# Optimization experiments

Measured on AMD Instinct MI355X. Metric: run time of the kernel, lower is better.

## Reference

```python
import jax, jax.numpy as jnp
import numpy as np
from jax import lax

B = 256; N_LAB = 20000; M = 3; D = 768
T = 5; K = 8; H = 256; DI = 512; S = 16; R = 16; NL = 4; KC = 4


def setup_inputs() -> dict:
    key = jax.random.key(0)
    ks = jax.random.split(key, 16)
    sc = 0.02
    return {
        "unlabeled_embeddings": jax.random.normal(ks[0], (B, M, D), jnp.float32),
        "labeled_embeddings": jax.random.normal(ks[1], (N_LAB, M, D), jnp.float32),
        "labeled_traits": jax.random.uniform(ks[2], (N_LAB, T), jnp.float32),
        "modality_logits": jax.random.normal(ks[3], (T, M), jnp.float32),
        "Wp": jax.random.normal(ks[4], (D + 1, H), jnp.float32) * sc,
        "bp": jnp.zeros((H,), jnp.float32),
        "ln_g": jnp.ones((NL, H), jnp.float32),
        "ln_b": jnp.zeros((NL, H), jnp.float32),
        "Win": jax.random.normal(ks[5], (NL, H, 2 * DI), jnp.float32) * sc,
        "conv_w": jax.random.normal(ks[6], (NL, DI, KC), jnp.float32) * sc,
        "conv_b": jnp.zeros((NL, DI), jnp.float32),
        "Wx": jax.random.normal(ks[7], (NL, DI, R + 2 * S), jnp.float32) * sc,
        "Wdt": jax.random.normal(ks[8], (NL, R, DI), jnp.float32) * sc,
        "bdt": jnp.full((NL, DI), -4.6, jnp.float32),
        "A_log": jnp.log(jnp.broadcast_to(jnp.arange(1, S + 1, dtype=jnp.float32), (NL, DI, S))),
        "Dp": jnp.ones((NL, DI), jnp.float32),
        "Wout": jax.random.normal(ks[9], (NL, DI, H), jnp.float32) * sc,
        "W1": jax.random.normal(ks[10], (H, H // 2), jnp.float32) * sc,
        "b1": jnp.zeros((H // 2,), jnp.float32),
        "W2": jax.random.normal(ks[11], (H // 2, 1), jnp.float32) * sc,
        "b2": jnp.zeros((1,), jnp.float32),
    }


def layer_norm(x, g, b, eps=1e-5):
    m = x.mean(-1, keepdims=True)
    v = ((x - m) ** 2).mean(-1, keepdims=True)
    return (x - m) * lax.rsqrt(v + eps) * g + b


def select_neighbors(lab_e, lab_t, unl_e, mlog):
    # Per-trait modality-weighted cosine similarity k-NN.
    w = jax.nn.softmax(mlog, axis=-1)                       # (T,M)
    q = jnp.einsum('tm,bmd->btd', w, unl_e)                 # (B,T,D)
    kk = jnp.einsum('tm,nmd->ntd', w, lab_e)                # (N,T,D)
    qn = q * lax.rsqrt(jnp.sum(q * q, -1, keepdims=True) + 1e-8)
    kn = kk * lax.rsqrt(jnp.sum(kk * kk, -1, keepdims=True) + 1e-8)
    sim = jnp.einsum('btd,ntd->btn', qn, kn)                # (B,T,N)
    _, idx = lax.top_k(sim, K)                              # (B,T,K) int32
    ne = lab_e[idx]                                         # (B,T,K,M,D)
    tg = lab_t[idx]                                         # (B,T,K,T)
    nt = jnp.diagonal(tg, axis1=1, axis2=3).transpose(0, 2, 1)  # (B,T,K)
    return ne, nt, idx


def mamba_block(x, Win, conv_w, conv_b, Wx, Wdt, bdt, A_log, Dp, Wout):
    # x: (N, L, H). Selective SSM (Mamba) block with internal residual.
    N, L, _ = x.shape
    xz = x @ Win                                            # (N,L,2*DI)
    xc, z = jnp.split(xz, 2, axis=-1)
    xp = jnp.pad(xc, ((0, 0), (KC - 1, 0), (0, 0)))         # causal depthwise conv, k=4
    xc = sum(xp[:, j:j + L, :] * conv_w[:, j] for j in range(KC)) + conv_b
    xc = jax.nn.silu(xc)
    dbl = xc @ Wx                                           # (N,L,R+2S)
    dt, Bm, Cm = jnp.split(dbl, [R, R + S], axis=-1)
    dt = jax.nn.softplus(dt @ Wdt + bdt)                    # (N,L,DI)
    A = -jnp.exp(A_log)                                     # (DI,S)
    dA = jnp.exp(dt[..., None] * A)                         # (N,L,DI,S)
    dBx = dt[..., None] * Bm[:, :, None, :] * xc[..., None] # (N,L,DI,S)

    def step(h, inp):
        a, bx = inp
        h = a * h + bx
        return h, h

    h0 = jnp.zeros((N, DI, S), x.dtype)
    _, hs = lax.scan(step, h0, (jnp.swapaxes(dA, 0, 1), jnp.swapaxes(dBx, 0, 1)))
    hs = jnp.swapaxes(hs, 0, 1)                             # (N,L,DI,S)
    y = jnp.einsum('nlds,nls->nld', hs, Cm) + Dp * xc
    y = y * jax.nn.silu(z)
    return x + y @ Wout


def _forward(unl, lab_e, lab_t, mlog, Wp, bp, ln_g, ln_b, Win, conv_w, conv_b, Wx,
             Wdt, bdt, A_log, Dp, Wout, W1, b1, W2, b2):
    ne, nt, _ = select_neighbors(lab_e, lab_t, unl, mlog)
    ne = ne.mean(3)                                         # (B,T,K,D) mean over modalities
    uc = unl.mean(1)                                        # (B,D)
    feats = jnp.concatenate([ne, jnp.broadcast_to(uc[:, None, None, :], (B, T, 1, D))], axis=2)
    tt = jnp.concatenate([nt[..., None], jnp.zeros((B, T, 1, 1), lab_t.dtype)], axis=2)
    toks = jnp.concatenate([feats, tt], axis=-1).reshape(B * T, K + 1, D + 1)
    x = toks @ Wp + bp                                      # (B*T, K+1, H)
    for i in range(NL):
        xn = layer_norm(x, ln_g[i], ln_b[i])
        x = mamba_block(xn, Win[i], conv_w[i], conv_b[i], Wx[i], Wdt[i], bdt[i],
                        A_log[i], Dp[i], Wout[i])
    ms = x[:, -1, :]                                        # masked-trait token state
    h1 = jax.nn.relu(ms @ W1 + b1)
    return (h1 @ W2 + b2).reshape(B, T)


def reference(unlabeled_embeddings, labeled_embeddings, labeled_traits, modality_logits,
              Wp, bp, ln_g, ln_b, Win, conv_w, conv_b, Wx, Wdt, bdt, A_log, Dp, Wout,
              W1, b1, W2, b2):
    return _forward(unlabeled_embeddings, labeled_embeddings, labeled_traits,
                    modality_logits, Wp, bp, ln_g, ln_b, Win, conv_w, conv_b, Wx,
                    Wdt, bdt, A_log, Dp, Wout, W1, b1, W2, b2)
```

## Files before the change

### kernel.cpp

```cpp
#include <hip/hip_runtime.h>
#include <math.h>

#define B_   256
#define NLAB 20000
#define M_   3
#define D_   768
#define T_   5
#define K_   8
#define H_   256
#define DI_  512
#define S_   16
#define R_   16
#define NL_  4
#define KC_  4
#define L_   9
#define NBT  1280
#define NROW 11520

typedef __attribute__((ext_vector_type(8))) short bf16x8;
typedef __attribute__((ext_vector_type(4))) float floatx4;


__device__ __forceinline__ float block_reduce_sum(float v) {
    __shared__ float red[4];
    int lane = threadIdx.x & 63;
    int wid  = threadIdx.x >> 6;
#pragma unroll
    for (int o = 32; o > 0; o >>= 1) v += __shfl_down(v, o);
    if (lane == 0) red[wid] = v;
    __syncthreads();
    int nw = (int)(blockDim.x >> 6);
    float r = 0.f;
#pragma unroll
    for (int i = 0; i < 4; ++i) if (i < nw) r += red[i];
    __syncthreads();
    return r;
}

__device__ __forceinline__ float sigmoidf_(float x) { return 1.f / (1.f + expf(-x)); }
__device__ __forceinline__ float siluf_(float x)    { return x * sigmoidf_(x); }
__device__ __forceinline__ float softplusf_(float x){ return x > 20.f ? x : log1pf(expf(x)); }

__device__ __forceinline__ unsigned short f2bf(float x) {
    unsigned u = __float_as_uint(x);
    unsigned r = (u + 0x7fffu + ((u >> 16) & 1u)) >> 16;
    return (unsigned short)r;
}
__device__ __forceinline__ float bf2f(unsigned short h) {
    return __uint_as_float(((unsigned)h) << 16);
}

__device__ __forceinline__ void barrier_lds_only() {
    asm volatile("s_waitcnt lgkmcnt(0)" ::: "memory");
    __builtin_amdgcn_s_barrier();
}


__global__ void k_softmax_w(const float* __restrict__ mlog, float* __restrict__ w) {
    int t = threadIdx.x;
    if (t < T_) {
        float a = mlog[t*M_+0], b = mlog[t*M_+1], c = mlog[t*M_+2];
        float mx = fmaxf(a, fmaxf(b, c));
        float ea = expf(a-mx), eb = expf(b-mx), ec = expf(c-mx);
        float s = ea + eb + ec;
        w[t*M_+0] = ea/s; w[t*M_+1] = eb/s; w[t*M_+2] = ec/s;
    }
}

__global__ __launch_bounds__(256) void k_qn_uc(const float* __restrict__ unl,
                                               const float* __restrict__ w,
                                               unsigned short* __restrict__ qnh,
                                               unsigned short* __restrict__ qnl,
                                               float* __restrict__ uc) {
    int b = blockIdx.x, tid = threadIdx.x;
    float e[3][3];
#pragma unroll
    for (int c = 0; c < 3; ++c) {
        int d = tid + c*256;
#pragma unroll
        for (int m = 0; m < 3; ++m)
            e[c][m] = unl[((size_t)b*3 + m)*D_ + d];
    }
#pragma unroll
    for (int c = 0; c < 3; ++c)
        uc[(size_t)b*D_ + tid + c*256] = (e[c][0] + e[c][1] + e[c][2]) * (1.f/3.f);
    for (int t = 0; t < T_; ++t) {
        float w0 = w[t*3+0], w1 = w[t*3+1], w2 = w[t*3+2];
        float q[3]; float ss = 0.f;
#pragma unroll
        for (int c = 0; c < 3; ++c) {
            q[c] = w0*e[c][0] + w1*e[c][1] + w2*e[c][2];
            ss += q[c]*q[c];
        }
        float tot = block_reduce_sum(ss);
        float inv = rsqrtf(tot + 1e-8f);
#pragma unroll
        for (int c = 0; c < 3; ++c) {
            float v = q[c]*inv;
            size_t o = ((size_t)t*B_ + b)*D_ + tid + c*256;
            unsigned short h = f2bf(v);
            qnh[o] = h; qnl[o] = f2bf(v - bf2f(h));
        }
    }
}

__device__ __forceinline__ void cvt_store4(const float4* rb, float w0, float w1, float w2,
                                           unsigned short* bh, unsigned short* bl,
                                           int off, float& ss) {
    float4 s;
    s.x = w0*rb[0].x + w1*rb[1].x + w2*rb[2].x;
    s.y = w0*rb[0].y + w1*rb[1].y + w2*rb[2].y;
    s.z = w0*rb[0].z + w1*rb[1].z + w2*rb[2].z;
    s.w = w0*rb[0].w + w1*rb[1].w + w2*rb[2].w;
    ss += s.x*s.x + s.y*s.y + s.z*s.z + s.w*s.w;
    ushort4 h, l;
    h.x = f2bf(s.x); l.x = f2bf(s.x - bf2f(h.x));
    h.y = f2bf(s.y); l.y = f2bf(s.y - bf2f(h.y));
    h.z = f2bf(s.z); l.z = f2bf(s.z - bf2f(h.z));
    h.w = f2bf(s.w); l.w = f2bf(s.w - bf2f(h.w));
    *(ushort4*)(bh + off) = h;
    *(ushort4*)(bl + off) = l;
}

__global__ __launch_bounds__(512, 4) void k_simf(const unsigned short* __restrict__ qnh,
                                                 const unsigned short* __restrict__ qnl,
                                                 const float* __restrict__ lab_e,
                                                 const float* __restrict__ w,
                                                 float* __restrict__ sim) {
    __shared__ unsigned short Ah[2][128*36], Al[2][128*36];
    __shared__ unsigned short Bh[2][128*36], Bl[2][128*36];
    __shared__ float rnl[128];

    int bid = blockIdx.x;
    int xcd = bid & 7, s = bid >> 3;
    int cnt = (xcd < 5) ? 20 : 19;
    if (s >= cnt * 10) return;
    int start = (xcd < 5) ? xcd*20 : 100 + (xcd - 5)*19;
    int chunk = start + s / 10;
    int inner = s - (s / 10) * 10;
    int mch = inner / 5;
    int t = inner - mch * 5;
    int bn = chunk * 128;
    int bm = mch * 128;

    float w0 = w[t*3+0], w1 = w[t*3+1], w2 = w[t*3+2];
    int tid = threadIdx.x;
    int lane = tid & 63, wv = tid >> 6;
    int mbase = (wv >> 2)*64, nbase = (wv & 3)*32;
    int fr = lane & 15, kg = lane >> 4;

    int ar = tid >> 2, akq = tid & 3;
    const unsigned short* agh = qnh + ((size_t)t*B_ + bm + ar)*D_ + akq*8;
    const unsigned short* agl = qnl + ((size_t)t*B_ + bm + ar)*D_ + akq*8;
    int aoff = ar*36 + akq*8;

    int gr0 = tid >> 3, gr1 = 64 + (tid >> 3), kq = tid & 7;
    int gn0 = bn + gr0, gn1 = bn + gr1;
    bool v0 = gn0 < NLAB, v1 = gn1 < NLAB;
    const float* bp0 = lab_e + (size_t)gn0*(3*D_) + kq*4;
    const float* bp1 = lab_e + (size_t)gn1*(3*D_) + kq*4;
    int soff0 = gr0*36 + kq*4, soff1 = gr1*36 + kq*4;

    floatx4 acc[4][2];
#pragma unroll
    for (int mi = 0; mi < 4; ++mi)
#pragma unroll
        for (int ni = 0; ni < 2; ++ni)
            acc[mi][ni] = (floatx4){0.f, 0.f, 0.f, 0.f};

    float ss0 = 0.f, ss1 = 0.f;
    float4 rb0[3], rb1[3];
    float4 z4 = make_float4(0.f, 0.f, 0.f, 0.f);
    int4 lah, lal;

    rb0[0]=rb0[1]=rb0[2]=z4; rb1[0]=rb1[1]=rb1[2]=z4;
    if (v0) { rb0[0] = *(const float4*)(bp0);
              rb0[1] = *(const float4*)(bp0 + D_);
              rb0[2] = *(const float4*)(bp0 + 2*D_); }
    if (v1) { rb1[0] = *(const float4*)(bp1);
              rb1[1] = *(const float4*)(bp1 + D_);
              rb1[2] = *(const float4*)(bp1 + 2*D_); }
    lah = *(const int4*)(agh);
    lal = *(const int4*)(agl);

    *(int4*)(&Ah[0][aoff]) = lah;
    *(int4*)(&Al[0][aoff]) = lal;
    cvt_store4(rb0, w0, w1, w2, &Bh[0][0], &Bl[0][0], soff0, ss0);
    cvt_store4(rb1, w0, w1, w2, &Bh[0][0], &Bl[0][0], soff1, ss1);

    if (v0) { rb0[0] = *(const float4*)(bp0 + 32);
              rb0[1] = *(const float4*)(bp0 + D_ + 32);
              rb0[2] = *(const float4*)(bp0 + 2*D_ + 32); }
    if (v1) { rb1[0] = *(const float4*)(bp1 + 32);
              rb1[1] = *(const float4*)(bp1 + D_ + 32);
              rb1[2] = *(const float4*)(bp1 + 2*D_ + 32); }
    lah = *(const int4*)(agh + 32);
    lal = *(const int4*)(agl + 32);

    for (int kt = 0; kt < 24; ++kt) {
        int cur = kt & 1;
        barrier_lds_only();

        bf16x8 bhf[2], blf[2];
#pragma unroll
        for (int ni = 0; ni < 2; ++ni) {
            int off = (nbase + ni*16 + fr)*36 + kg*8;
            bhf[ni] = *(const bf16x8*)(&Bh[cur][off]);
            blf[ni] = *(const bf16x8*)(&Bl[cur][off]);
        }
#pragma unroll
        for (int mi = 0; mi < 4; ++mi) {
            int off = (mbase + mi*16 + fr)*36 + kg*8;
            bf16x8 ahf = *(const bf16x8*)(&Ah[cur][off]);
            bf16x8 alf = *(const bf16x8*)(&Al[cur][off]);
#pragma unroll
            for (int ni = 0; ni < 2; ++ni) {
                floatx4 c = acc[mi][ni];
                c = __builtin_amdgcn_mfma_f32_16x16x32_bf16(ahf, bhf[ni], c, 0, 0, 0);
                c = __builtin_amdgcn_mfma_f32_16x16x32_bf16(alf, bhf[ni], c, 0, 0, 0);
                c = __builtin_amdgcn_mfma_f32_16x16x32_bf16(ahf, blf[ni], c, 0, 0, 0);
                acc[mi][ni] = c;
            }
        }
        if (kt < 23) {
            int nxt = cur ^ 1;
            *(int4*)(&Ah[nxt][aoff]) = lah;
            *(int4*)(&Al[nxt][aoff]) = lal;
            cvt_store4(rb0, w0, w1, w2, &Bh[nxt][0], &Bl[nxt][0], soff0, ss0);
            cvt_store4(rb1, w0, w1, w2, &Bh[nxt][0], &Bl[nxt][0], soff1, ss1);
            if (kt < 22) {
                int k2 = (kt + 2) * 32;
                if (v0) { rb0[0] = *(const float4*)(bp0 + k2);
                          rb0[1] = *(const float4*)(bp0 + D_ + k2);
                          rb0[2] = *(const float4*)(bp0 + 2*D_ + k2); }
                if (v1) { rb1[0] = *(const float4*)(bp1 + k2);
                          rb1[1] = *(const float4*)(bp1 + D_ + k2);
                          rb1[2] = *(const float4*)(bp1 + 2*D_ + k2); }
                lah = *(const int4*)(agh + k2);
                lal = *(const int4*)(agl + k2);
            }
        }
    }

    float t0 = ss0, t1 = ss1;
#pragma unroll
    for (int m = 1; m <= 4; m <<= 1) { t0 += __shfl_xor(t0, m); t1 += __shfl_xor(t1, m); }
    if ((tid & 7) == 0) {
        rnl[tid >> 3]        = rsqrtf(t0 + 1e-8f);
        rnl[64 + (tid >> 3)] = rsqrtf(t1 + 1e-8f);
    }
    __syncthreads();

    float* st = sim + (size_t)t*B_*NLAB;
#pragma unroll
    for (int mi = 0; mi < 4; ++mi) {
        int m = bm + mbase + mi*16 + kg*4;
#pragma unroll
        for (int ni = 0; ni < 2; ++ni) {
            int nl = nbase + ni*16 + fr;
            int n = bn + nl;
            if (n < NLAB) {
                float rv = rnl[nl];
#pragma unroll
                for (int r2 = 0; r2 < 4; ++r2)
                    st[(size_t)(m + r2)*NLAB + n] = acc[mi][ni][r2] * rv;
            }
        }
    }
}

__global__ __launch_bounds__(256) void k_topk(const float* __restrict__ sim,
                                              int* __restrict__ idx_out) {
    int b = blockIdx.x;
    int t = blockIdx.y;
    int tid = threadIdx.x;
    const float* row = sim + ((size_t)t*B_ + b)*NLAB;
    float tv[8]; int ti[8];
#pragma unroll
    for (int k = 0; k < 8; ++k) { tv[k] = -3e38f; ti[k] = 0x7fffffff; }
    for (int n = tid; n < NLAB; n += 256) {
        float v = row[n];
        if (v > tv[7]) {
            tv[7] = v; ti[7] = n;
#pragma unroll
            for (int k = 7; k > 0; --k) {
                if (tv[k] > tv[k-1]) {
                    float fv = tv[k]; tv[k] = tv[k-1]; tv[k-1] = fv;
                    int fi = ti[k]; ti[k] = ti[k-1]; ti[k-1] = fi;
                }
            }
        }
    }
    __shared__ float sv[2048];
    __shared__ int   si[2048];
    __shared__ float pv[256];
    __shared__ int   pi[256];
    __shared__ int   pp[256];
#pragma unroll
    for (int k = 0; k < 8; ++k) { sv[tid*8+k] = tv[k]; si[tid*8+k] = ti[k]; }
    __syncthreads();
    for (int r = 0; r < 8; ++r) {
        float bv = -3e38f; int bi = 0x7fffffff; int bp = 0;
#pragma unroll
        for (int k = 0; k < 8; ++k) {
            int p = tid*8 + k;
            float v = sv[p]; int ii = si[p];
            if (v > bv || (v == bv && ii < bi)) { bv = v; bi = ii; bp = p; }
        }
        pv[tid] = bv; pi[tid] = bi; pp[tid] = bp;
        __syncthreads();
        for (int off = 128; off > 0; off >>= 1) {
            if (tid < off) {
                if (pv[tid+off] > pv[tid] || (pv[tid+off] == pv[tid] && pi[tid+off] < pi[tid])) {
                    pv[tid] = pv[tid+off]; pi[tid] = pi[tid+off]; pp[tid] = pp[tid+off];
                }
            }
            __syncthreads();
        }
        if (tid == 0) {
            idx_out[((size_t)b*T_ + t)*K_ + r] = pi[0];
            sv[pp[0]] = -3e38f;
        }
        __syncthreads();
    }
}

__global__ __launch_bounds__(256) void k_toks(const float* __restrict__ lab_e,
                                              const float* __restrict__ lab_t,
                                              const float* __restrict__ uc,
                                              const int* __restrict__ idx,
                                              unsigned short* __restrict__ tokh,
                                              unsigned short* __restrict__ tokl,
                                              float* __restrict__ tt) {
    int g = blockIdx.x;
    int bt = g / L_, l = g % L_;
    int b = bt / T_, t = bt % T_;
    size_t ro = (size_t)g*D_;
    if (l < K_) {
        int n = idx[(size_t)bt*K_ + l];
        for (int d = threadIdx.x; d < D_; d += 256) {
            size_t base = (size_t)n*(3*D_) + d;
            float v = (lab_e[base] + lab_e[base + D_] + lab_e[base + 2*D_]) * (1.f/3.f);
            unsigned short h = f2bf(v);
            tokh[ro + d] = h; tokl[ro + d] = f2bf(v - bf2f(h));
        }
        if (threadIdx.x == 0) tt[g] = lab_t[(size_t)n*T_ + t];
    } else {
        for (int d = threadIdx.x; d < D_; d += 256) {
            float v = uc[(size_t)b*D_ + d];
            unsigned short h = f2bf(v);
            tokh[ro + d] = h; tokl[ro + d] = f2bf(v - bf2f(h));
        }
        if (threadIdx.x == 0) tt[g] = 0.f;
    }
}

__global__ void k_cvtw(const float* __restrict__ W,
                       unsigned short* __restrict__ th,
                       unsigned short* __restrict__ tl,
                       int Kd, int N) {
    int total = Kd * N;
    for (int id = blockIdx.x*256 + threadIdx.x; id < total; id += gridDim.x*256) {
        int n = id / Kd, k = id - n*Kd;
        float v = W[(size_t)k*N + n];
        unsigned short h = f2bf(v);
        th[id] = h; tl[id] = f2bf(v - bf2f(h));
    }
}

template<bool ADD, bool BIAS, bool TRAIT>
__global__ __launch_bounds__(256) void k_mgemm(const unsigned short* __restrict__ ah,
                                               const unsigned short* __restrict__ al,
                                               const unsigned short* __restrict__ bh,
                                               const unsigned short* __restrict__ bl,
                                               const float* __restrict__ bias,
                                               const float* __restrict__ wtrait,
                                               const float* __restrict__ tt,
                                               float* __restrict__ C,
                                               int N, int Kd) {
    __shared__ unsigned short Ah[128*40], Al[128*40], Bh[64*40], Bl[64*40];
    int bn = blockIdx.x * 64;
    int bm = blockIdx.y * 128;
    int tid = threadIdx.x;
    int lane = tid & 63, wv = tid >> 6;
    int mbase = (wv >> 1)*64, nbase = (wv & 1)*32;
    int fr = lane & 15, kg = lane >> 4;
    floatx4 acc[4][2];
#pragma unroll
    for (int mi = 0; mi < 4; ++mi)
#pragma unroll
        for (int ni = 0; ni < 2; ++ni)
            acc[mi][ni] = (floatx4){0.f, 0.f, 0.f, 0.f};

    for (int k0 = 0; k0 < Kd; k0 += 32) {
#pragma unroll
        for (int f = 0; f < 2; ++f) {
            int v = f*256 + tid;
            int r = v >> 2, kq = v & 3;
            size_t g = (size_t)(bm + r)*Kd + k0 + kq*8;
            int off = r*40 + kq*8;
            *(int4*)(Ah + off) = *(const int4*)(ah + g);
            *(int4*)(Al + off) = *(const int4*)(al + g);
        }
        {
            int r = tid >> 2, kq = tid & 3;
            size_t g = (size_t)(bn + r)*Kd + k0 + kq*8;
            int off = r*40 + kq*8;
            *(int4*)(Bh + off) = *(const int4*)(bh + g);
            *(int4*)(Bl + off) = *(const int4*)(bl + g);
        }
        __syncthreads();

        bf16x8 bhf[2], blf[2];
#pragma unroll
        for (int ni = 0; ni < 2; ++ni) {
            int off = (nbase + ni*16 + fr)*40 + kg*8;
            bhf[ni] = *(const bf16x8*)(Bh + off);
            blf[ni] = *(const bf16x8*)(Bl + off);
        }
#pragma unroll
        for (int mi = 0; mi < 4; ++mi) {
            int off = (mbase + mi*16 + fr)*40 + kg*8;
            bf16x8 ahf = *(const bf16x8*)(Ah + off);
            bf16x8 alf = *(const bf16x8*)(Al + off);
#pragma unroll
            for (int ni = 0; ni < 2; ++ni) {
                floatx4 c = acc[mi][ni];
                c = __builtin_amdgcn_mfma_f32_16x16x32_bf16(ahf, bhf[ni], c, 0, 0, 0);
                c = __builtin_amdgcn_mfma_f32_16x16x32_bf16(alf, bhf[ni], c, 0, 0, 0);
                c = __builtin_amdgcn_mfma_f32_16x16x32_bf16(ahf, blf[ni], c, 0, 0, 0);
                acc[mi][ni] = c;
            }
        }
        __syncthreads();
    }
#pragma unroll
    for (int mi = 0; mi < 4; ++mi) {
        int m0 = bm + mbase + mi*16 + kg*4;
#pragma unroll
        for (int ni = 0; ni < 2; ++ni) {
            int n = bn + nbase + ni*16 + fr;
#pragma unroll
            for (int r = 0; r < 4; ++r) {
                float v = acc[mi][ni][r];
                if (TRAIT) v += tt[m0 + r] * wtrait[n];
                if (BIAS)  v += bias[n];
                size_t o = (size_t)(m0 + r)*N + n;
                if (ADD) C[o] += v; else C[o] = v;
            }
        }
    }
}

__global__ __launch_bounds__(256) void k_ln(const float* __restrict__ x,
                                            const float* __restrict__ g,
                                            const float* __restrict__ b,
                                            float* __restrict__ xn,
                                            unsigned short* __restrict__ xnh,
                                            unsigned short* __restrict__ xnl) {
    int row = blockIdx.x, tid = threadIdx.x;
    float v = x[(size_t)row*H_ + tid];
    float mean = block_reduce_sum(v) * (1.f/H_);
    float d = v - mean;
    float var = block_reduce_sum(d*d) * (1.f/H_);
    float o = d * rsqrtf(var + 1e-5f) * g[tid] + b[tid];
    size_t oo = (size_t)row*H_ + tid;
    xn[oo] = o;
    unsigned short h = f2bf(o);
    xnh[oo] = h; xnl[oo] = f2bf(o - bf2f(h));
}

__global__ __launch_bounds__(512) void k_mamba(const float* __restrict__ xz,
                                               const float* __restrict__ cw,
                                               const float* __restrict__ cb,
                                               const unsigned short* __restrict__ wxh,
                                               const unsigned short* __restrict__ wxl,
                                               const float* __restrict__ Wdt,
                                               const float* __restrict__ bdt,
                                               const float* __restrict__ A_log,
                                               const float* __restrict__ Dp,
                                               unsigned short* __restrict__ yh,
                                               unsigned short* __restrict__ yl) {
    __shared__ float xcS[L_][516];
    __shared__ float dblS[L_][48];
    int n = blockIdx.x, d = threadIdx.x;

    float c0 = cw[d*4+0], c1 = cw[d*4+1], c2 = cw[d*4+2], c3 = cw[d*4+3];
    float bb = cb[d];
    const float* src = xz + (size_t)n*L_*(2*DI_) + d;
    float xc[L_], z[L_];
    float x0 = 0.f, x1 = 0.f, x2 = 0.f;
#pragma unroll
    for (int l = 0; l < L_; ++l) {
        float x3 = src[l*(2*DI_)];
        z[l]     = src[l*(2*DI_) + DI_];
        float s = bb + c0*x0 + c1*x1 + c2*x2 + c3*x3;
        float v = siluf_(s);
        xc[l] = v; xcS[l][d] = v;
        x0 = x1; x1 = x2; x2 = x3;
    }
    __syncthreads();

    int wv = d >> 6, lane = d & 63;
    if (wv < 3) {
        int fr = lane & 15, kg = lane >> 4;
        const unsigned short* bph = wxh + (size_t)(wv*16 + fr)*DI_;
        const unsigned short* bpl = wxl + (size_t)(wv*16 + fr)*DI_;
        floatx4 c = (floatx4){0.f, 0.f, 0.f, 0.f};
        for (int k0 = 0; k0 < DI_; k0 += 32) {
            int kb = k0 + kg*8;
            float av[8];
            if (fr < L_) {
                float4 q0 = *(const float4*)(&xcS[fr][kb]);
                float4 q1 = *(const float4*)(&xcS[fr][kb+4]);
                av[0]=q0.x; av[1]=q0.y; av[2]=q0.z; av[3]=q0.w;
                av[4]=q1.x; av[5]=q1.y; av[6]=q1.z; av[7]=q1.w;
            } else {
#pragma unroll
                for (int j = 0; j < 8; ++j) av[j] = 0.f;
            }
            bf16x8 ah, al;
#pragma unroll
            for (int j = 0; j < 8; ++j) {
                unsigned short hh = f2bf(av[j]);
                ah[j] = (short)hh;
                al[j] = (short)f2bf(av[j] - bf2f(hh));
            }
            bf16x8 bhf = *(const bf16x8*)(bph + kb);
            bf16x8 blf = *(const bf16x8*)(bpl + kb);
            c = __builtin_amdgcn_mfma_f32_16x16x32_bf16(ah, bhf, c, 0, 0, 0);
            c = __builtin_amdgcn_mfma_f32_16x16x32_bf16(al, bhf, c, 0, 0, 0);
            c = __builtin_amdgcn_mfma_f32_16x16x32_bf16(ah, blf, c, 0, 0, 0);
        }
#pragma unroll
        for (int r = 0; r < 4; ++r) {
            int row = kg*4 + r;
            if (row < L_) dblS[row][wv*16 + fr] = c[r];
        }
    }
    __syncthreads();

    float a[S_], wdt[R_];
#pragma unroll
    for (int s = 0; s < S_; ++s) a[s] = -expf(A_log[(size_t)d*S_ + s]);
#pragma unroll
    for (int r = 0; r < R_; ++r) wdt[r] = Wdt[(size_t)r*DI_ + d];
    float bdtv = bdt[d], dp = Dp[d];
    float h[S_];
#pragma unroll
    for (int s = 0; s < S_; ++s) h[s] = 0.f;
    size_t ob = (size_t)n*L_*DI_ + d;
#pragma unroll
    for (int l = 0; l < L_; ++l) {
        float s = bdtv;
#pragma unroll
        for (int r = 0; r < R_; ++r) s = fmaf(dblS[l][r], wdt[r], s);
        float dtv = softplusf_(s);
        float xcv = xc[l];
        float accv = 0.f;
#pragma unroll
        for (int si = 0; si < S_; ++si) {
            float Bv = dblS[l][16 + si], Cv = dblS[l][32 + si];
            h[si] = expf(dtv*a[si])*h[si] + dtv*Bv*xcv;
            accv = fmaf(h[si], Cv, accv);
        }
        float yv = (accv + dp*xcv) * siluf_(z[l]);
        unsigned short hh = f2bf(yv);
        yh[ob + (size_t)l*DI_] = hh;
        yl[ob + (size_t)l*DI_] = f2bf(yv - bf2f(hh));
    }
}

__global__ __launch_bounds__(128) void k_head(const float* __restrict__ x,
                                              const float* __restrict__ W1,
                                              const float* __restrict__ b1,
                                              const float* __restrict__ W2,
                                              const float* __restrict__ b2,
                                              float* __restrict__ out) {
    int n = blockIdx.x, tid = threadIdx.x;
    __shared__ float ms[H_];
    const float* src = x + ((size_t)n*L_ + (L_-1))*H_;
    ms[tid] = src[tid];
    ms[tid+128] = src[tid+128];
    __syncthreads();
    float s = b1[tid];
#pragma unroll 8
    for (int k = 0; k < H_; ++k) s = fmaf(ms[k], W1[(size_t)k*128 + tid], s);
    float h = fmaxf(s, 0.f);
    float p = h * W2[tid];
    float tot = block_reduce_sum(p);
    if (tid == 0) out[n] = tot + b2[0];
}


extern "C" void kernel_launch(void* const* d_in, const int* in_sizes, int n_in,
                              void* d_out, int out_size, void* d_ws, size_t ws_size,
                              hipStream_t stream) {
    const float* unl   = (const float*)d_in[0];
    const float* lab_e = (const float*)d_in[1];
    const float* lab_t = (const float*)d_in[2];
    const float* mlog  = (const float*)d_in[3];
    const float* Wp    = (const float*)d_in[4];
    const float* bp    = (const float*)d_in[5];
    const float* ln_g  = (const float*)d_in[6];
    const float* ln_b  = (const float*)d_in[7];
    const float* Win   = (const float*)d_in[8];
    const float* conv_w= (const float*)d_in[9];
    const float* conv_b= (const float*)d_in[10];
    const float* Wx    = (const float*)d_in[11];
    const float* Wdt   = (const float*)d_in[12];
    const float* bdt   = (const float*)d_in[13];
    const float* A_log = (const float*)d_in[14];
    const float* Dp    = (const float*)d_in[15];
    const float* Wout  = (const float*)d_in[16];
    const float* W1    = (const float*)d_in[17];
    const float* b1    = (const float*)d_in[18];
    const float* W2    = (const float*)d_in[19];
    const float* b2    = (const float*)d_in[20];

    float* ws = (float*)d_ws;
    float* w    = ws + 0;
    int*   idx  = (int*)(ws + 16);
    float* uc   = ws + 10256;
    unsigned short* wxth = (unsigned short*)(ws + 206864);
    unsigned short* wxtl = (unsigned short*)(ws + 256016);
    float* tt   = ws + 306864;
    unsigned short* qnh   = (unsigned short*)(ws + 318384);
    unsigned short* qnl   = (unsigned short*)(ws + 809904);
    unsigned short* wph   = (unsigned short*)(ws + 1301424);
    unsigned short* wpl   = (unsigned short*)(ws + 1399728);
    unsigned short* winh  = (unsigned short*)(ws + 1498032);
    unsigned short* winl  = (unsigned short*)(ws + 2022320);
    unsigned short* wouth = (unsigned short*)(ws + 2546608);
    unsigned short* woutl = (unsigned short*)(ws + 2808752);
    float* xa   = ws + 3070896;
    float* xb   = ws + 6020016;
    unsigned short* xnh   = (unsigned short*)(ws + 8969136);
    unsigned short* xnl   = (unsigned short*)(ws + 10443696);
    float* simreg = ws + 18369456;
    float* sim  = simreg;
    float* xz   = simreg;
    unsigned short* tokh = (unsigned short*)(simreg + 11796480);
    unsigned short* tokl = (unsigned short*)(simreg + 16220160);
    unsigned short* yh   = (unsigned short*)(simreg + 17694720);
    unsigned short* yl   = (unsigned short*)(simreg + 20643840);

    k_softmax_w<<<1, 64, 0, stream>>>(mlog, w);
    k_qn_uc<<<B_, 256, 0, stream>>>(unl, w, qnh, qnl, uc);
    k_cvtw<<<(768*256 + 255)/256, 256, 0, stream>>>(Wp, wph, wpl, 768, 256);
    for (int i = 0; i < NL_; ++i) {
        k_cvtw<<<(256*1024 + 255)/256, 256, 0, stream>>>(Win + (size_t)i*H_*(2*DI_),
                                                         winh + (size_t)i*H_*(2*DI_),
                                                         winl + (size_t)i*H_*(2*DI_), 256, 1024);
        k_cvtw<<<(512*256 + 255)/256, 256, 0, stream>>>(Wout + (size_t)i*DI_*H_,
                                                        wouth + (size_t)i*DI_*H_,
                                                        woutl + (size_t)i*DI_*H_, 512, 256);
        k_cvtw<<<(512*48 + 255)/256, 256, 0, stream>>>(Wx + (size_t)i*DI_*48,
                                                       wxth + (size_t)i*48*DI_,
                                                       wxtl + (size_t)i*48*DI_, 512, 48);
    }
    k_simf<<<1600, 512, 0, stream>>>(qnh, qnl, lab_e, w, sim);
    {
        dim3 g(B_, T_);
        k_topk<<<g, 256, 0, stream>>>(sim, idx);
    }
    k_toks<<<NROW, 256, 0, stream>>>(lab_e, lab_t, uc, idx, tokh, tokl, tt);
    {
        dim3 g(H_/64, NROW/128);
        k_mgemm<false,true,true><<<g, 256, 0, stream>>>(tokh, tokl, wph, wpl,
                                                        bp, Wp + (size_t)768*H_, tt, xa, H_, D_);
    }
    float* cur = xa;
    float* oth = xb;
    for (int i = 0; i < NL_; ++i) {
        k_ln<<<NROW, 256, 0, stream>>>(cur, ln_g + (size_t)i*H_, ln_b + (size_t)i*H_, oth, xnh, xnl);
        {
            dim3 g((2*DI_)/64, NROW/128);
            k_mgemm<false,false,false><<<g, 256, 0, stream>>>(xnh, xnl,
                winh + (size_t)i*H_*(2*DI_), winl + (size_t)i*H_*(2*DI_),
                nullptr, nullptr, nullptr, xz, 2*DI_, H_);
        }
        k_mamba<<<NBT, 512, 0, stream>>>(xz,
                                         conv_w + (size_t)i*DI_*KC_, conv_b + (size_t)i*DI_,
                                         wxth + (size_t)i*48*DI_, wxtl + (size_t)i*48*DI_,
                                         Wdt + (size_t)i*R_*DI_, bdt + (size_t)i*DI_,
                                         A_log + (size_t)i*DI_*S_, Dp + (size_t)i*DI_,
                                         yh, yl);
        {
            dim3 g(H_/64, NROW/128);
            k_mgemm<true,false,false><<<g, 256, 0, stream>>>(yh, yl,
                wouth + (size_t)i*DI_*H_, woutl + (size_t)i*DI_*H_,
                nullptr, nullptr, nullptr, oth, H_, DI_);
        }
        float* tmp = cur; cur = oth; oth = tmp;
    }
    k_head<<<NBT, 128, 0, stream>>>(cur, W1, b1, W2, b2, (float*)d_out);
}
```

Before: 1.417 ms.

## Single-buffer LDS in similarity GEMM, pad rows to 40, raise occupancy

Replaces the double-buffered LDS tiles in the similarity GEMM with a single buffer and adds a second barrier per k-step, so the next tile's stores happen before compute rather than overlapping it. LDS row stride changes from 36 to 40 halves and launch bounds ask for 8 blocks per CU instead of 4. The bf16 conversions now use the compiler's native __bf16 cast. The aim is higher occupancy from the smaller LDS footprint, paid for with an extra barrier per k-step, less overlap inside each block, and possible register pressure at the higher occupancy target.

```diff
diff --git a/kernel.cpp b/kernel.cpp
--- a/kernel.cpp
+++ b/kernel.cpp
@@ -42,12 +42,10 @@
 __device__ __forceinline__ float softplusf_(float x){ return x > 20.f ? x : log1pf(expf(x)); }
 
 __device__ __forceinline__ unsigned short f2bf(float x) {
-    unsigned u = __float_as_uint(x);
-    unsigned r = (u + 0x7fffu + ((u >> 16) & 1u)) >> 16;
-    return (unsigned short)r;
+    return __builtin_bit_cast(unsigned short, (__bf16)x);
 }
 __device__ __forceinline__ float bf2f(unsigned short h) {
-    return __uint_as_float(((unsigned)h) << 16);
+    return (float)__builtin_bit_cast(__bf16, h);
 }
 
 __device__ __forceinline__ void barrier_lds_only() {
@@ -122,22 +120,22 @@
     *(ushort4*)(bl + off) = l;
 }
 
-__global__ __launch_bounds__(512, 4) void k_simf(const unsigned short* __restrict__ qnh,
+__global__ __launch_bounds__(512, 8) void k_simf(const unsigned short* __restrict__ qnh,
                                                  const unsigned short* __restrict__ qnl,
                                                  const float* __restrict__ lab_e,
                                                  const float* __restrict__ w,
                                                  float* __restrict__ sim) {
-    __shared__ unsigned short Ah[2][128*36], Al[2][128*36];
-    __shared__ unsigned short Bh[2][128*36], Bl[2][128*36];
+    __shared__ unsigned short Ah[128*40], Al[128*40];
+    __shared__ unsigned short Bh[128*40], Bl[128*40];
     __shared__ float rnl[128];
 
     int bid = blockIdx.x;
-    int xcd = bid & 7, s = bid >> 3;
+    int xcd = bid & 7, sb = bid >> 3;
     int cnt = (xcd < 5) ? 20 : 19;
-    if (s >= cnt * 10) return;
+    if (sb >= cnt * 10) return;
     int start = (xcd < 5) ? xcd*20 : 100 + (xcd - 5)*19;
-    int chunk = start + s / 10;
-    int inner = s - (s / 10) * 10;
+    int chunk = start + sb / 10;
+    int inner = sb - (sb / 10) * 10;
     int mch = inner / 5;
     int t = inner - mch * 5;
     int bn = chunk * 128;
@@ -152,14 +150,14 @@
     int ar = tid >> 2, akq = tid & 3;
     const unsigned short* agh = qnh + ((size_t)t*B_ + bm + ar)*D_ + akq*8;
     const unsigned short* agl = qnl + ((size_t)t*B_ + bm + ar)*D_ + akq*8;
-    int aoff = ar*36 + akq*8;
+    int aoff = ar*40 + akq*8;
 
     int gr0 = tid >> 3, gr1 = 64 + (tid >> 3), kq = tid & 7;
     int gn0 = bn + gr0, gn1 = bn + gr1;
     bool v0 = gn0 < NLAB, v1 = gn1 < NLAB;
     const float* bp0 = lab_e + (size_t)gn0*(3*D_) + kq*4;
     const float* bp1 = lab_e + (size_t)gn1*(3*D_) + kq*4;
-    int soff0 = gr0*36 + kq*4, soff1 = gr1*36 + kq*4;
+    int soff0 = gr0*40 + kq*4, soff1 = gr1*40 + kq*4;
 
     floatx4 acc[4][2];
 #pragma unroll
@@ -183,36 +181,40 @@
     lah = *(const int4*)(agh);
     lal = *(const int4*)(agl);
 
-    *(int4*)(&Ah[0][aoff]) = lah;
-    *(int4*)(&Al[0][aoff]) = lal;
-    cvt_store4(rb0, w0, w1, w2, &Bh[0][0], &Bl[0][0], soff0, ss0);
-    cvt_store4(rb1, w0, w1, w2, &Bh[0][0], &Bl[0][0], soff1, ss1);
-
-    if (v0) { rb0[0] = *(const float4*)(bp0 + 32);
-              rb0[1] = *(const float4*)(bp0 + D_ + 32);
-              rb0[2] = *(const float4*)(bp0 + 2*D_ + 32); }
-    if (v1) { rb1[0] = *(const float4*)(bp1 + 32);
-              rb1[1] = *(const float4*)(bp1 + D_ + 32);
-              rb1[2] = *(const float4*)(bp1 + 2*D_ + 32); }
-    lah = *(const int4*)(agh + 32);
-    lal = *(const int4*)(agl + 32);
-
     for (int kt = 0; kt < 24; ++kt) {
-        int cur = kt & 1;
         barrier_lds_only();
 
+        *(int4*)(&Ah[aoff]) = lah;
+        *(int4*)(&Al[aoff]) = lal;
+        cvt_store4(rb0, w0, w1, w2, Bh, Bl, soff0, ss0);
+        cvt_store4(rb1, w0, w1, w2, Bh, Bl, soff1, ss1);
+
+        if (kt < 23) {
+            int k2 = (kt + 1) * 32;
+            if (v0) { rb0[0] = *(const float4*)(bp0 + k2);
+                      rb0[1] = *(const float4*)(bp0 + D_ + k2);
+                      rb0[2] = *(const float4*)(bp0 + 2*D_ + k2); }
+            if (v1) { rb1[0] = *(const float4*)(bp1 + k2);
+                      rb1[1] = *(const float4*)(bp1 + D_ + k2);
+                      rb1[2] = *(const float4*)(bp1 + 2*D_ + k2); }
+            lah = *(const int4*)(agh + k2);
+            lal = *(const int4*)(agl + k2);
+        }
+
+        barrier_lds_only();
+
         bf16x8 bhf[2], blf[2];
 #pragma unroll
         for (int ni = 0; ni < 2; ++ni) {
-            int off = (nbase + ni*16 + fr)*36 + kg*8;
-            bhf[ni] = *(const bf16x8*)(&Bh[cur][off]);
-            blf[ni] = *(const bf16x8*)(&Bl[cur][off]);
+            int off = (nbase + ni*16 + fr)*40 + kg*8;
+            bhf[ni] = *(const bf16x8*)(Bh + off);
+            blf[ni] = *(const bf16x8*)(Bl + off);
         }
 #pragma unroll
         for (int mi = 0; mi < 4; ++mi) {
-            int off = (mbase + mi*16 + fr)*36 + kg*8;
-            bf16x8 ahf = *(const bf16x8*)(&Ah[cur][off]);
-            bf16x8 alf = *(const bf16x8*)(&Al[cur][off]);
+            int off = (mbase + mi*16 + fr)*40 + kg*8;
+            bf16x8 ahf = *(const bf16x8*)(Ah + off);
+            bf16x8 alf = *(const bf16x8*)(Al + off);
 #pragma unroll
             for (int ni = 0; ni < 2; ++ni) {
                 floatx4 c = acc[mi][ni];
@@ -220,24 +222,6 @@
                 c = __builtin_amdgcn_mfma_f32_16x16x32_bf16(alf, bhf[ni], c, 0, 0, 0);
                 c = __builtin_amdgcn_mfma_f32_16x16x32_bf16(ahf, blf[ni], c, 0, 0, 0);
                 acc[mi][ni] = c;
-            }
-        }
-        if (kt < 23) {
-            int nxt = cur ^ 1;
-            *(int4*)(&Ah[nxt][aoff]) = lah;
-            *(int4*)(&Al[nxt][aoff]) = lal;
-            cvt_store4(rb0, w0, w1, w2, &Bh[nxt][0], &Bl[nxt][0], soff0, ss0);
-            cvt_store4(rb1, w0, w1, w2, &Bh[nxt][0], &Bl[nxt][0], soff1, ss1);
-            if (kt < 22) {
-                int k2 = (kt + 2) * 32;
-                if (v0) { rb0[0] = *(const float4*)(bp0 + k2);
-                          rb0[1] = *(const float4*)(bp0 + D_ + k2);
-                          rb0[2] = *(const float4*)(bp0 + 2*D_ + k2); }
-                if (v1) { rb1[0] = *(const float4*)(bp1 + k2);
-                          rb1[1] = *(const float4*)(bp1 + D_ + k2);
-                          rb1[2] = *(const float4*)(bp1 + 2*D_ + k2); }
-                lah = *(const int4*)(agh + k2);
-                lal = *(const int4*)(agl + k2);
             }
         }
     }
```

New measurement: 1.392 ms. About the same (-1.8%).
